# Kernel optimization log

Measured on AMD Instinct MI355X. Metric: run time of the kernel, lower is better.

## Reference

```python
import jax, jax.numpy as jnp
import numpy as np

B, S, HID = 2, 2048, 2048
H, HKV, HD = 16, 4, 128  # heads, kv heads, head_dim; n_rep = H // HKV


def rotate_half(x):
    h = x.shape[-1] // 2
    return jnp.concatenate((-x[..., h:], x[..., :h]), axis=-1)


def setup_inputs() -> dict:
    key = jax.random.key(0)
    ks = jax.random.split(key, 7)
    sc = 0.02
    return {
        "x": jax.random.normal(ks[0], (B, S, HID), jnp.float32),
        "cos": jax.random.uniform(ks[1], (S, HD), jnp.float32),
        "sin": jax.random.uniform(ks[2], (S, HD), jnp.float32),
        "wq": jax.random.normal(ks[3], (H * HD, HID), jnp.float32) * sc,
        "wk": jax.random.normal(ks[4], (HKV * HD, HID), jnp.float32) * sc,
        "wv": jax.random.normal(ks[5], (HKV * HD, HID), jnp.float32) * sc,
        "wo": jax.random.normal(ks[6], (HID, H * HD), jnp.float32) * sc,
    }


def reference(x, cos, sin, wq, wk, wv, wo):
    bs, seq_len, _ = x.shape
    n_rep = H // HKV

    # projections (Linear with weight [out, in]: y = x @ W.T)
    q = (x @ wq.T).reshape(bs, seq_len, H, HD)
    k = (x @ wk.T).reshape(bs, seq_len, HKV, HD)
    v = (x @ wv.T).reshape(bs, seq_len, HKV, HD)

    # RoPE: cos/sin [S, HD] -> broadcast over heads (unsqueeze_dim=1 after seq)
    c = cos[:seq_len][:, None, :]  # [S,1,HD]
    s = sin[:seq_len][:, None, :]
    q = q * c + rotate_half(q) * s
    k = k * c + rotate_half(k) * s

    # repeat KV heads (GQA) and move heads forward: [b,h,s,d]
    k = jnp.repeat(k, n_rep, axis=2).transpose(0, 2, 1, 3)
    v = jnp.repeat(v, n_rep, axis=2).transpose(0, 2, 1, 3)
    q = q.transpose(0, 2, 1, 3)

    # causal SDPA
    scale = 1.0 / jnp.sqrt(jnp.float32(HD))
    scores = jnp.einsum("bhqd,bhkd->bhqk", q, k) * scale
    causal = jnp.tril(jnp.ones((seq_len, seq_len), bool))
    scores = jnp.where(causal, scores, jnp.float32(-jnp.inf))
    probs = jax.nn.softmax(scores, axis=-1)
    out = jnp.einsum("bhqk,bhkd->bhqd", probs, v)

    out = out.transpose(0, 2, 1, 3).reshape(bs, seq_len, H * HD)
    return out @ wo.T
```

## Files before the change

kernel.cpp:

```cpp
#include <hip/hip_runtime.h>
#include <hip/hip_bf16.h>
#include <math.h>

#define B_    2
#define S_    2048
#define HID_  2048
#define H_    16
#define HKV_  4
#define HD_   128
#define BS_   (B_*S_)
#define QSTRIDE 3072
#define L2E 1.4426950408889634f

typedef __attribute__((ext_vector_type(8))) short bf16x8;
typedef __attribute__((ext_vector_type(4))) float f32x4;
typedef __attribute__((ext_vector_type(16))) float f32x16;
typedef unsigned int uint;

typedef __attribute__((address_space(3))) void lds_void;
typedef __attribute__((address_space(1))) const void gbl_cvoid;

__device__ __forceinline__ void load_lds16(const void* g, void* l) {
  __builtin_amdgcn_global_load_lds((gbl_cvoid*)g, (lds_void*)l, 16, 0, 0);
}

__device__ __forceinline__ unsigned short f2bf(float f) {
  uint u = __float_as_uint(f);
  u = (u + 0x7fff + ((u >> 16) & 1)) >> 16;
  return (unsigned short)u;
}
__device__ __forceinline__ float bf2f(unsigned short u) {
  return __uint_as_float(((uint)u) << 16);
}
__device__ __forceinline__ uint cvtpk_bf16(float lo, float hi) {
  uint r;
  asm("v_cvt_pk_bf16_f32 %0, %1, %2" : "=v"(r) : "v"(lo), "v"(hi));
  return r;
}
__device__ __forceinline__ void swap32(uint& a, uint& b) {
  asm("v_permlane32_swap_b32 %0, %1" : "+v"(a), "+v"(b));
}

__global__ __launch_bounds__(256) void cast_f32_bf16(
    const float* __restrict__ src, unsigned short* __restrict__ dst, int n)
{
  int i = (blockIdx.x * 256 + threadIdx.x) * 4;
  if (i < n) {
    float4 v = *(const float4*)(src + i);
    ushort4 o;
    o.x = f2bf(v.x); o.y = f2bf(v.y); o.z = f2bf(v.z); o.w = f2bf(v.w);
    *(ushort4*)(dst + i) = o;
  }
}

template <int BN, int WRITE_BF16>
__global__ __launch_bounds__(512, 2) void gemm_nt_8ph(
    const unsigned short* __restrict__ A, const unsigned short* __restrict__ W,
    void* __restrict__ Cv, int M, int N, int K)
{
  constexpr int ASLAB = 16384;
  constexpr int BSLAB = BN * 64;
  constexpr int ABUF  = 2 * ASLAB;
  constexpr int BBUF  = 2 * BSLAB;
  constexpr int RN    = BN / 4;
  constexpr int NTN   = RN / 16;

  __shared__ __align__(16) char lds_[2 * ABUF + 2 * BBUF];
  char* const AL = lds_;
  char* const BL = lds_ + 2 * ABUF;

  const int tid = threadIdx.x;
  const int lane = tid & 63;
  const int wid = tid >> 6;
  const int wm = wid >> 2, wn = wid & 3;
  const int c_ = lane & 15, g4 = lane >> 4;
  const int bm = blockIdx.y * 256, bn = blockIdx.x * BN;

  const size_t rs = (size_t)K * 2;
  const char* Ag = (const char*)A + (size_t)bm * rs;
  const char* Bg = (const char*)W + (size_t)bn * rs;

  const int stq = tid >> 2;
  const int stslot = ((tid & 3) ^ (stq & 3)) * 16;
  const int fsl = (g4 ^ (c_ & 3)) << 4;
  const int dst = tid * 16;

  f32x4 acc[2][4][NTN];
#pragma unroll
  for (int mh = 0; mh < 2; ++mh)
#pragma unroll
    for (int mt = 0; mt < 4; ++mt)
#pragma unroll
      for (int nt = 0; nt < NTN; ++nt) acc[mh][mt][nt] = (f32x4){0.f, 0.f, 0.f, 0.f};

  const int NT = K / 64;

  auto stA = [&](char* buf, int slab, int half, int kbyte) {
    load_lds16(Ag + (size_t)(half * 128 + stq) * rs + kbyte + stslot,
               buf + slab * ASLAB + half * 8192 + dst);
  };
  auto stB = [&](char* buf, int slab, int half, int kbyte) {
    load_lds16(Bg + (size_t)(half * 128 + stq) * rs + kbyte + stslot,
               buf + slab * BSLAB + half * 8192 + dst);
  };

  stA(AL, 0, 0, 0); stB(BL, 0, 0, 0); stA(AL, 0, 1, 0);
  if constexpr (BN == 256) stB(BL, 0, 1, 0);
  stA(AL, 1, 0, 64); stB(BL, 1, 0, 64); stA(AL, 1, 1, 64);
  if constexpr (BN == 256) stB(BL, 1, 1, 64);

  const int afb = (wm * 128 + c_) * 64 + fsl;
  const int bfb = (wn * RN + c_) * 64 + fsl;

#define WAITK do { if constexpr (BN == 256) asm volatile("s_waitcnt vmcnt(4)" ::: "memory"); \
                   else                     asm volatile("s_waitcnt vmcnt(3)" ::: "memory"); \
                   __builtin_amdgcn_s_barrier(); \
                   __builtin_amdgcn_sched_barrier(0); } while (0)

  for (int t = 0; t < NT; ++t) {
    const char* Ac = AL + (t & 1) * ABUF;
    const char* Bc = BL + (t & 1) * BBUF;
    char* An = AL + ((t + 1) & 1) * ABUF;
    char* Bn = BL + ((t + 1) & 1) * BBUF;
    const int tn = (t + 1 < NT) ? t + 1 : 0;
    const int kb = tn * 128;

    WAITK;

    bf16x8 af[4], bf0[NTN];

#pragma unroll
    for (int mt = 0; mt < 4; ++mt)
      af[mt] = *(const bf16x8*)(Ac + afb + mt * 1024);
#pragma unroll
    for (int nt = 0; nt < NTN; ++nt)
      bf0[nt] = *(const bf16x8*)(Bc + bfb + nt * 1024);
    stA(An, 0, 0, kb); stB(Bn, 0, 0, kb);
    __builtin_amdgcn_s_setprio(1);
#pragma unroll
    for (int mt = 0; mt < 4; ++mt)
#pragma unroll
      for (int nt = 0; nt < NTN; ++nt)
        acc[0][mt][nt] = __builtin_amdgcn_mfma_f32_16x16x32_bf16(af[mt], bf0[nt], acc[0][mt][nt], 0, 0, 0);
    __builtin_amdgcn_s_setprio(0);

#pragma unroll
    for (int mt = 0; mt < 4; ++mt)
      af[mt] = *(const bf16x8*)(Ac + afb + 4096 + mt * 1024);
    stA(An, 0, 1, kb);
    if constexpr (BN == 256) stB(Bn, 0, 1, kb);
    __builtin_amdgcn_s_setprio(1);
#pragma unroll
    for (int mt = 0; mt < 4; ++mt)
#pragma unroll
      for (int nt = 0; nt < NTN; ++nt)
        acc[1][mt][nt] = __builtin_amdgcn_mfma_f32_16x16x32_bf16(af[mt], bf0[nt], acc[1][mt][nt], 0, 0, 0);
    __builtin_amdgcn_s_setprio(0);

    WAITK;

#pragma unroll
    for (int mt = 0; mt < 4; ++mt)
      af[mt] = *(const bf16x8*)(Ac + ASLAB + afb + mt * 1024);
#pragma unroll
    for (int nt = 0; nt < NTN; ++nt)
      bf0[nt] = *(const bf16x8*)(Bc + BSLAB + bfb + nt * 1024);
    stA(An, 1, 0, kb + 64); stB(Bn, 1, 0, kb + 64);
    __builtin_amdgcn_s_setprio(1);
#pragma unroll
    for (int mt = 0; mt < 4; ++mt)
#pragma unroll
      for (int nt = 0; nt < NTN; ++nt)
        acc[0][mt][nt] = __builtin_amdgcn_mfma_f32_16x16x32_bf16(af[mt], bf0[nt], acc[0][mt][nt], 0, 0, 0);
    __builtin_amdgcn_s_setprio(0);

#pragma unroll
    for (int mt = 0; mt < 4; ++mt)
      af[mt] = *(const bf16x8*)(Ac + ASLAB + afb + 4096 + mt * 1024);
    stA(An, 1, 1, kb + 64);
    if constexpr (BN == 256) stB(Bn, 1, 1, kb + 64);
    __builtin_amdgcn_s_setprio(1);
#pragma unroll
    for (int mt = 0; mt < 4; ++mt)
#pragma unroll
      for (int nt = 0; nt < NTN; ++nt)
        acc[1][mt][nt] = __builtin_amdgcn_mfma_f32_16x16x32_bf16(af[mt], bf0[nt], acc[1][mt][nt], 0, 0, 0);
    __builtin_amdgcn_s_setprio(0);
  }
#undef WAITK

#pragma unroll
  for (int mh = 0; mh < 2; ++mh)
#pragma unroll
    for (int mt = 0; mt < 4; ++mt)
#pragma unroll
      for (int r = 0; r < 4; ++r) {
        size_t row = bm + wm * 128 + mh * 64 + mt * 16 + g4 * 4 + r;
#pragma unroll
        for (int nt = 0; nt < NTN; ++nt) {
          size_t col = bn + wn * RN + nt * 16 + c_;
          float v = acc[mh][mt][nt][r];
          if (WRITE_BF16)
            ((unsigned short*)Cv)[row * N + col] = f2bf(v);
          else
            ((float*)Cv)[row * N + col] = v;
        }
      }
}

template <int NH, int LOGNH, int ROWE, int SCALE>
__global__ __launch_bounds__(256) void rope_bf16(
    unsigned short* __restrict__ p, const float* __restrict__ cosb,
    const float* __restrict__ sinb)
{
  int idx = blockIdx.x * 256 + threadIdx.x;
  int d = idx & 63;
  int h = (idx >> 6) & (NH - 1);
  int s = (idx >> (6 + LOGNH)) & (S_ - 1);
  int b = idx >> (6 + LOGNH + 11);

  size_t off = ((size_t)b * S_ + s) * ROWE + h * HD_ + d;
  float x1 = bf2f(p[off]);
  float x2 = bf2f(p[off + 64]);
  float c1 = cosb[s * HD_ + d],      s1 = sinb[s * HD_ + d];
  float c2 = cosb[s * HD_ + d + 64], s2 = sinb[s * HD_ + d + 64];
  float o1 = x1 * c1 - x2 * s1;
  float o2 = x2 * c2 + x1 * s2;
  if (SCALE) { o1 *= 0.08838834764831845f; o2 *= 0.08838834764831845f; }
  p[off]      = f2bf(o1);
  p[off + 64] = f2bf(o2);
}

__global__ __launch_bounds__(256) void attn_fwd_bf16(
    const unsigned short* __restrict__ QKV, unsigned short* __restrict__ O)
{
  __shared__ __align__(16) char lds[65536];

  const int tid = threadIdx.x;
  const int lane = tid & 63;
  const int wq = tid >> 6;
  const int ql = lane & 31;
  const int hi = lane >> 5;

  const int bid = blockIdx.x;
  const int halfg = bid >> 8, rem = bid & 255;
  const int bh = rem >> 3, a2 = rem & 7;
  const int qt = halfg ? (15 - 2 * a2) : (2 * a2);
  const int b = bh >> 4, h = bh & 15, kh = h >> 2;
  const int q0 = qt * 128;
  const int qglob = q0 + wq * 32 + ql;
  const int ktmax_w = (q0 + wq * 32 + 31) >> 6;
  const int ntiles = 2 * qt + 2;

  bf16x8 qf[8];
  {
    const unsigned short* qsrc =
        QKV + ((size_t)(b * S_) + qglob) * QSTRIDE + h * HD_ + hi * 8;
#pragma unroll
    for (int ds = 0; ds < 8; ++ds) qf[ds] = *(const bf16x8*)(qsrc + ds * 16);
  }

  f32x16 acc[4];
#pragma unroll
  for (int dt = 0; dt < 4; ++dt)
#pragma unroll
    for (int r = 0; r < 16; ++r) acc[dt][r] = 0.f;
  float m_ = -3.0e38f, l_ = 0.f;

  const char* Kg = (const char*)(QKV + (size_t)b * S_ * QSTRIDE + 2048 + kh * HD_);
  const unsigned short* Vg = QKV + (size_t)b * S_ * QSTRIDE + 2560 + kh * HD_;

  const int dc = tid & 15;
  const int kq4 = (tid >> 4) * 4;
  bf16x8 vr[4];

#pragma unroll
  for (int p = 0; p < 4; ++p) {
    int db = p * 4096 + tid * 16;
    int row = db >> 8;
    int cb = (db & 255) ^ ((row & 7) << 4);
    load_lds16(Kg + (size_t)row * (QSTRIDE * 2) + cb, lds + db);
  }
  {
    const unsigned short* vs = Vg + (size_t)kq4 * QSTRIDE + dc * 8;
#pragma unroll
    for (int i = 0; i < 4; ++i) vr[i] = *(const bf16x8*)(vs + i * QSTRIDE);
#pragma unroll
    for (int s = 0; s < 8; ++s) {
      int j = (dc + s) & 7;
      int d = dc * 8 + j;
      uint w0 = (uint)(unsigned short)vr[0][j] | ((uint)(unsigned short)vr[1][j] << 16);
      uint w1 = (uint)(unsigned short)vr[2][j] | ((uint)(unsigned short)vr[3][j] << 16);
      *(uint2*)(lds + 32768 + d * 128 + ((kq4 * 2) ^ (j << 4))) = make_uint2(w0, w1);
    }
  }
  __syncthreads();

  for (int kt = 0; kt < ntiles; ++kt) {
    const int cur = kt & 1;
    const bool pf = (kt + 1 < ntiles);

    if (pf) {
#pragma unroll
      for (int p = 0; p < 4; ++p) {
        int db = p * 4096 + tid * 16;
        int row = db >> 8;
        int cb = (db & 255) ^ ((row & 7) << 4);
        load_lds16(Kg + (size_t)((kt + 1) * 64 + row) * (QSTRIDE * 2) + cb,
                   lds + (cur ^ 1) * 16384 + db);
      }
      const unsigned short* vs = Vg + (size_t)((kt + 1) * 64 + kq4) * QSTRIDE + dc * 8;
#pragma unroll
      for (int i = 0; i < 4; ++i) vr[i] = *(const bf16x8*)(vs + i * QSTRIDE);
    }

    if (kt <= ktmax_w) {
      const char* ksc = lds + cur * 16384;
      const char* vtc = lds + 32768 + cur * 16384;
#pragma unroll
      for (int ks2 = 0; ks2 < 2; ++ks2) {
        f32x16 s;
#pragma unroll
        for (int r = 0; r < 16; ++r) s[r] = 0.f;
        const int kk = ks2 * 32 + ql;
        const char* krow = ksc + kk * 256;
        const int ksw = (kk & 7) << 4;
#pragma unroll
        for (int ds = 0; ds < 8; ++ds) {
          bf16x8 kf = *(const bf16x8*)(krow + ((ds * 32 + hi * 16) ^ ksw));
          s = __builtin_amdgcn_mfma_f32_32x32x16_bf16(kf, qf[ds], s, 0, 0, 0);
        }

        if (kt == ktmax_w) {
          const int kb = kt * 64 + ks2 * 32 + 4 * hi;
#pragma unroll
          for (int r = 0; r < 16; ++r) {
            int kg = kb + (r & 3) + 8 * (r >> 2);
            if (kg > qglob) s[r] = -3.0e38f;
          }
        }

        float mx = s[0];
#pragma unroll
        for (int r = 1; r < 16; ++r) mx = fmaxf(mx, s[r]);
        mx = fmaxf(mx, __shfl_xor(mx, 32));
        const bool nd = mx > m_ + 8.f;
        float fr = 1.f;
        if (__any(nd)) {
          float mn = nd ? mx : m_;
          fr = nd ? exp2f((m_ - mn) * L2E) : 1.f;
          m_ = mn;
#pragma unroll
          for (int dt = 0; dt < 4; ++dt)
#pragma unroll
            for (int r = 0; r < 16; ++r) acc[dt][r] *= fr;
        }
        float pr[16];
        float sum = 0.f;
#pragma unroll
        for (int r = 0; r < 16; ++r) {
          pr[r] = exp2f((s[r] - m_) * L2E);
          sum += pr[r];
        }
        sum += __shfl_xor(sum, 32);
        l_ = l_ * fr + sum;

        uint wA0 = cvtpk_bf16(pr[0], pr[1]);
        uint wA1 = cvtpk_bf16(pr[2], pr[3]);
        uint wB0 = cvtpk_bf16(pr[4], pr[5]);
        uint wB1 = cvtpk_bf16(pr[6], pr[7]);
        swap32(wA0, wB0);
        swap32(wA1, wB1);
        uint wC0 = cvtpk_bf16(pr[8], pr[9]);
        uint wC1 = cvtpk_bf16(pr[10], pr[11]);
        uint wD0 = cvtpk_bf16(pr[12], pr[13]);
        uint wD1 = cvtpk_bf16(pr[14], pr[15]);
        swap32(wC0, wD0);
        swap32(wC1, wD1);
        union { uint u[4]; bf16x8 v; } p0, p1;
        p0.u[0] = wA0; p0.u[1] = wA1; p0.u[2] = wB0; p0.u[3] = wB1;
        p1.u[0] = wC0; p1.u[1] = wC1; p1.u[2] = wD0; p1.u[3] = wD1;

#pragma unroll
        for (int dt = 0; dt < 4; ++dt) {
          const int dr = dt * 32 + ql;
          const char* vrow = vtc + dr * 128;
          const int vsw = (dr & 7) << 4;
          bf16x8 v0 = *(const bf16x8*)(vrow + ((ks2 * 64 + hi * 16) ^ vsw));
          acc[dt] = __builtin_amdgcn_mfma_f32_32x32x16_bf16(v0, p0.v, acc[dt], 0, 0, 0);
          bf16x8 v1 = *(const bf16x8*)(vrow + ((ks2 * 64 + 32 + hi * 16) ^ vsw));
          acc[dt] = __builtin_amdgcn_mfma_f32_32x32x16_bf16(v1, p1.v, acc[dt], 0, 0, 0);
        }
      }
    }

    if (pf) {
#pragma unroll
      for (int s = 0; s < 8; ++s) {
        int j = (dc + s) & 7;
        int d = dc * 8 + j;
        uint w0 = (uint)(unsigned short)vr[0][j] | ((uint)(unsigned short)vr[1][j] << 16);
        uint w1 = (uint)(unsigned short)vr[2][j] | ((uint)(unsigned short)vr[3][j] << 16);
        *(uint2*)(lds + 32768 + (cur ^ 1) * 16384 + d * 128 + ((kq4 * 2) ^ (j << 4))) =
            make_uint2(w0, w1);
      }
    }
    __syncthreads();
  }

  {
    const float inv = 1.f / l_;
    char* wsc = lds + wq * 8704;
#pragma unroll
    for (int dt = 0; dt < 4; ++dt) {
#pragma unroll
      for (int i = 0; i < 8; ++i) {
        uint wv = cvtpk_bf16(acc[dt][2 * i] * inv, acc[dt][2 * i + 1] * inv);
        int d = 2 * (i & 1) + 8 * (i >> 1) + 4 * hi + 32 * dt;
        *(uint*)(wsc + ql * 272 + d * 2) = wv;
      }
    }
#pragma unroll
    for (int j = 0; j < 8; ++j) {
      bf16x8 ov = *(const bf16x8*)(wsc + ql * 272 + hi * 128 + j * 16);
      unsigned short* ob = O + ((size_t)(b * S_) + q0 + wq * 32 + ql) * (H_ * HD_) +
                           h * HD_ + hi * 64 + j * 8;
      *(bf16x8*)ob = ov;
    }
  }
}

extern "C" void kernel_launch(void* const* d_in, const int* in_sizes, int n_in,
                              void* d_out, int out_size, void* d_ws, size_t ws_size,
                              hipStream_t stream) {
  const float* x    = (const float*)d_in[0];
  const float* cosb = (const float*)d_in[1];
  const float* sinb = (const float*)d_in[2];
  const float* wq   = (const float*)d_in[3];
  const float* wk   = (const float*)d_in[4];
  const float* wv   = (const float*)d_in[5];
  const float* wo   = (const float*)d_in[6];
  float* out        = (float*)d_out;

  unsigned short* xb     = (unsigned short*)d_ws;
  unsigned short* wqkvb  = xb + 8388608;
  unsigned short* wob    = wqkvb + 6291456;
  unsigned short* qkv    = wob + 4194304;
  unsigned short* attnb  = qkv + 12582912;

  dim3 blk(256);

  cast_f32_bf16<<<8192, blk, 0, stream>>>(x, xb, 8388608);
  cast_f32_bf16<<<4096, blk, 0, stream>>>(wq, wqkvb, 4194304);
  cast_f32_bf16<<<1024, blk, 0, stream>>>(wk, wqkvb + 4194304, 1048576);
  cast_f32_bf16<<<1024, blk, 0, stream>>>(wv, wqkvb + 5242880, 1048576);
  cast_f32_bf16<<<4096, blk, 0, stream>>>(wo, wob, 4194304);

  gemm_nt_8ph<256, 1><<<dim3(12, 16), dim3(512), 0, stream>>>(
      xb, wqkvb, qkv, BS_, QSTRIDE, HID_);

  rope_bf16<16, 4, QSTRIDE, 1><<<16384, blk, 0, stream>>>(qkv, cosb, sinb);
  rope_bf16<4, 2, QSTRIDE, 0><<<4096, blk, 0, stream>>>(qkv + 2048, cosb, sinb);

  attn_fwd_bf16<<<512, blk, 0, stream>>>(qkv, attnb);

  gemm_nt_8ph<128, 0><<<dim3(16, 16), dim3(512), 0, stream>>>(
      attnb, wob, out, BS_, HID_, HID_);
}
```

Measured before the change: 345.4 us.

## Issue GEMM prefetch earlier and remap workgroups across XCDs

The GEMM main loop now issues all global-to-LDS loads for each next-stage slab at the top of the phase, before the LDS fragment reads, and uses deeper vmcnt waits mid-iteration, so more memory traffic is in flight during MFMA work. Workgroup IDs are also remapped so that consecutive tiles land on the same XCD (flat&7 striding), which should improve L2 reuse of A/B panels. An explicit vmcnt(0) drains outstanding loads before the epilogue. The cost is higher outstanding-load pressure and reliance on the assumption that the grid size is divisible by 8.

After: 353.3 us. 2.3% more time.

```diff
diff --git a/kernel.cpp b/kernel.cpp
--- a/kernel.cpp
+++ b/kernel.cpp
@@ -54,7 +54,7 @@
 }
 
 template <int BN, int WRITE_BF16>
-__global__ __launch_bounds__(512, 2) void gemm_nt_8ph(
+__global__ __launch_bounds__(512, 2) void gemm_nt_dp(
     const unsigned short* __restrict__ A, const unsigned short* __restrict__ W,
     void* __restrict__ Cv, int M, int N, int K)
 {
@@ -74,7 +74,12 @@
   const int wid = tid >> 6;
   const int wm = wid >> 2, wn = wid & 3;
   const int c_ = lane & 15, g4 = lane >> 4;
-  const int bm = blockIdx.y * 256, bn = blockIdx.x * BN;
+
+  const int gx = gridDim.x;
+  const int nwg = gx * gridDim.y;
+  const int flat = blockIdx.y * gx + blockIdx.x;
+  const int tile = (flat & 7) * (nwg >> 3) + (flat >> 3);
+  const int bm = (tile / gx) * 256, bn = (tile % gx) * BN;
 
   const size_t rs = (size_t)K * 2;
   const char* Ag = (const char*)A + (size_t)bm * rs;
@@ -104,18 +109,22 @@
                buf + slab * BSLAB + half * 8192 + dst);
   };
 
-  stA(AL, 0, 0, 0); stB(BL, 0, 0, 0); stA(AL, 0, 1, 0);
+  stA(AL, 0, 0, 0); stA(AL, 0, 1, 0); stB(BL, 0, 0, 0);
   if constexpr (BN == 256) stB(BL, 0, 1, 0);
-  stA(AL, 1, 0, 64); stB(BL, 1, 0, 64); stA(AL, 1, 1, 64);
+  stA(AL, 1, 0, 64); stA(AL, 1, 1, 64); stB(BL, 1, 0, 64);
   if constexpr (BN == 256) stB(BL, 1, 1, 64);
 
   const int afb = (wm * 128 + c_) * 64 + fsl;
   const int bfb = (wn * RN + c_) * 64 + fsl;
 
-#define WAITK do { if constexpr (BN == 256) asm volatile("s_waitcnt vmcnt(4)" ::: "memory"); \
-                   else                     asm volatile("s_waitcnt vmcnt(3)" ::: "memory"); \
-                   __builtin_amdgcn_s_barrier(); \
-                   __builtin_amdgcn_sched_barrier(0); } while (0)
+#define WAIT_TOP do { if constexpr (BN == 256) asm volatile("s_waitcnt vmcnt(4)" ::: "memory"); \
+                      else                     asm volatile("s_waitcnt vmcnt(3)" ::: "memory"); \
+                      __builtin_amdgcn_s_barrier(); \
+                      __builtin_amdgcn_sched_barrier(0); } while (0)
+#define WAIT_MID do { if constexpr (BN == 256) asm volatile("s_waitcnt vmcnt(8)" ::: "memory"); \
+                      else                     asm volatile("s_waitcnt vmcnt(6)" ::: "memory"); \
+                      __builtin_amdgcn_s_barrier(); \
+                      __builtin_amdgcn_sched_barrier(0); } while (0)
 
   for (int t = 0; t < NT; ++t) {
     const char* Ac = AL + (t & 1) * ABUF;
@@ -125,7 +134,10 @@
     const int tn = (t + 1 < NT) ? t + 1 : 0;
     const int kb = tn * 128;
 
-    WAITK;
+    WAIT_TOP;
+
+    stA(An, 0, 0, kb); stA(An, 0, 1, kb); stB(Bn, 0, 0, kb);
+    if constexpr (BN == 256) stB(Bn, 0, 1, kb);
 
     bf16x8 af[4], bf0[NTN];
 
@@ -135,7 +147,6 @@
 #pragma unroll
     for (int nt = 0; nt < NTN; ++nt)
       bf0[nt] = *(const bf16x8*)(Bc + bfb + nt * 1024);
-    stA(An, 0, 0, kb); stB(Bn, 0, 0, kb);
     __builtin_amdgcn_s_setprio(1);
 #pragma unroll
     for (int mt = 0; mt < 4; ++mt)
@@ -144,11 +155,12 @@
         acc[0][mt][nt] = __builtin_amdgcn_mfma_f32_16x16x32_bf16(af[mt], bf0[nt], acc[0][mt][nt], 0, 0, 0);
     __builtin_amdgcn_s_setprio(0);
 
+    stA(An, 1, 0, kb + 64); stA(An, 1, 1, kb + 64); stB(Bn, 1, 0, kb + 64);
+    if constexpr (BN == 256) stB(Bn, 1, 1, kb + 64);
+
 #pragma unroll
     for (int mt = 0; mt < 4; ++mt)
       af[mt] = *(const bf16x8*)(Ac + afb + 4096 + mt * 1024);
-    stA(An, 0, 1, kb);
-    if constexpr (BN == 256) stB(Bn, 0, 1, kb);
     __builtin_amdgcn_s_setprio(1);
 #pragma unroll
     for (int mt = 0; mt < 4; ++mt)
@@ -157,7 +169,7 @@
         acc[1][mt][nt] = __builtin_amdgcn_mfma_f32_16x16x32_bf16(af[mt], bf0[nt], acc[1][mt][nt], 0, 0, 0);
     __builtin_amdgcn_s_setprio(0);
 
-    WAITK;
+    WAIT_MID;
 
 #pragma unroll
     for (int mt = 0; mt < 4; ++mt)
@@ -165,7 +177,6 @@
 #pragma unroll
     for (int nt = 0; nt < NTN; ++nt)
       bf0[nt] = *(const bf16x8*)(Bc + BSLAB + bfb + nt * 1024);
-    stA(An, 1, 0, kb + 64); stB(Bn, 1, 0, kb + 64);
     __builtin_amdgcn_s_setprio(1);
 #pragma unroll
     for (int mt = 0; mt < 4; ++mt)
@@ -177,8 +188,6 @@
 #pragma unroll
     for (int mt = 0; mt < 4; ++mt)
       af[mt] = *(const bf16x8*)(Ac + ASLAB + afb + 4096 + mt * 1024);
-    stA(An, 1, 1, kb + 64);
-    if constexpr (BN == 256) stB(Bn, 1, 1, kb + 64);
     __builtin_amdgcn_s_setprio(1);
 #pragma unroll
     for (int mt = 0; mt < 4; ++mt)
@@ -187,7 +196,10 @@
         acc[1][mt][nt] = __builtin_amdgcn_mfma_f32_16x16x32_bf16(af[mt], bf0[nt], acc[1][mt][nt], 0, 0, 0);
     __builtin_amdgcn_s_setprio(0);
   }
-#undef WAITK
+#undef WAIT_TOP
+#undef WAIT_MID
+
+  asm volatile("s_waitcnt vmcnt(0)" ::: "memory");
 
 #pragma unroll
   for (int mh = 0; mh < 2; ++mh)
@@ -456,7 +468,7 @@
   cast_f32_bf16<<<1024, blk, 0, stream>>>(wv, wqkvb + 5242880, 1048576);
   cast_f32_bf16<<<4096, blk, 0, stream>>>(wo, wob, 4194304);
 
-  gemm_nt_8ph<256, 1><<<dim3(12, 16), dim3(512), 0, stream>>>(
+  gemm_nt_dp<256, 1><<<dim3(12, 16), dim3(512), 0, stream>>>(
       xb, wqkvb, qkv, BS_, QSTRIDE, HID_);
 
   rope_bf16<16, 4, QSTRIDE, 1><<<16384, blk, 0, stream>>>(qkv, cosb, sinb);
@@ -464,6 +476,6 @@
 
   attn_fwd_bf16<<<512, blk, 0, stream>>>(qkv, attnb);
 
-  gemm_nt_8ph<128, 0><<<dim3(16, 16), dim3(512), 0, stream>>>(
+  gemm_nt_dp<128, 0><<<dim3(16, 16), dim3(512), 0, stream>>>(
       attnb, wob, out, BS_, HID_, HID_);
 }
```
